# Kernel tuning notes

Hardware: AMD Instinct MI355X
Metric: run time of the kernel (lower is better)

The kernel has to match this reference:

```python
import jax, jax.numpy as jnp
import numpy as np

B, T, D, DFF, H, L, E, HID, GOUT = 64, 16, 2048, 2048, 8, 2, 32, 64, 32
THRESH = 0.05
MAXENT = float(np.log(7.0))

# per-sample edge template over 9 node slots: 0=phase, 1=location, 2..8=lesion k
_pairs = [(0, 1), (1, 0)]
for _k in range(7):
    _pairs += [(1, 2 + _k), (2 + _k, 1)]
for _i in range(7):
    for _j in range(_i + 1, 7):
        _pairs += [(2 + _i, 2 + _j), (2 + _j, 2 + _i)]
SRC_L = np.array([p[0] for p in _pairs], np.int32)  # [58]
DST_L = np.array([p[1] for p in _pairs], np.int32)


def _layernorm(x, g, b):
    m = x.mean(-1, keepdims=True)
    v = ((x - m) ** 2).mean(-1, keepdims=True)
    return (x - m) * jax.lax.rsqrt(v + 1e-5) * g + b


def setup_inputs():
    key = jax.random.key(0)
    ks = iter(jax.random.split(key, 32))
    def w(shape, s=0.02):
        return jax.random.normal(next(ks), shape, dtype=jnp.float32) * s
    return {
        'feat': jax.random.normal(next(ks), (B * T, D), dtype=jnp.float32),
        'w_phase': w((D, 3)), 'b_phase': jnp.zeros((3,), jnp.float32),
        'w_loc': w((D, 7)), 'b_loc': jnp.zeros((7,), jnp.float32),
        'w_les': w((D, 7)), 'b_les': jnp.zeros((7,), jnp.float32),
        'emb_phase': w((3, E), 1.0), 'emb_loc': w((7, E), 1.0),
        'les_emb_w': w((7, E), 0.2), 'les_emb_b': jnp.zeros((E,), jnp.float32),
        'qkv_w': w((L, 3 * D, D)), 'qkv_b': jnp.zeros((L, 3 * D), jnp.float32),
        'o_w': w((L, D, D)), 'o_b': jnp.zeros((L, D), jnp.float32),
        'ln1_g': jnp.ones((L, D), jnp.float32), 'ln1_b': jnp.zeros((L, D), jnp.float32),
        'ln2_g': jnp.ones((L, D), jnp.float32), 'ln2_b': jnp.zeros((L, D), jnp.float32),
        'ff1_w': w((L, DFF, D)), 'ff1_b': jnp.zeros((L, DFF), jnp.float32),
        'ff2_w': w((L, D, DFF)), 'ff2_b': jnp.zeros((L, D), jnp.float32),
        'w_score': w((D,)), 'b_score': jnp.zeros((1,), jnp.float32),
        'gcn1_w': w((E, HID), 0.2), 'gcn1_b': jnp.zeros((HID,), jnp.float32),
        'gcn2_w': w((HID, GOUT), 0.2), 'gcn2_b': jnp.zeros((GOUT,), jnp.float32),
        'w_diag': w((D + GOUT, 7)), 'b_diag': jnp.zeros((7,), jnp.float32),
        'mask': jax.random.randint(next(ks), (B, T), 0, 2, dtype=jnp.int32),
    }


def _forward(feat, w_phase, b_phase, w_loc, b_loc, w_les, b_les, emb_phase, emb_loc,
             les_emb_w, les_emb_b, qkv_w, qkv_b, o_w, o_b, ln1_g, ln1_b, ln2_g, ln2_b,
             ff1_w, ff1_b, ff2_w, ff2_b, w_score, b_score, gcn1_w, gcn1_b, gcn2_w,
             gcn2_b, w_diag, b_diag, mask):
    S = B * T
    Dh = D // H
    maskb = mask.astype(bool)            # [B,T]
    mflat = maskb.reshape(S)

    # per-frame heads
    phase_logits = feat @ w_phase + b_phase    # [S,3]
    loc_logits = feat @ w_loc + b_loc          # [S,7]
    les_logits = feat @ w_les + b_les          # [S,7]
    phase_ids = jnp.argmax(phase_logits, -1)
    loc_ids = jnp.argmax(loc_logits, -1)
    les_act = jax.nn.sigmoid(les_logits) > 0.5  # [S,7]

    # transformer encoder: 2 post-norm layers, eval mode (dropout off)
    x = feat.reshape(B, T, D)
    kp = maskb[:, None, None, :]
    for l in range(L):
        qkv = x @ qkv_w[l].T + qkv_b[l]
        q, k, v = jnp.split(qkv, 3, axis=-1)
        q = q.reshape(B, T, H, Dh)
        k = k.reshape(B, T, H, Dh)
        v = v.reshape(B, T, H, Dh)
        s = jnp.einsum('bqhd,bkhd->bhqk', q, k) / np.sqrt(Dh)
        s = jnp.where(kp, s, -1e9)
        a = jax.nn.softmax(s, axis=-1)
        ctx = jnp.einsum('bhqk,bkhd->bqhd', a, v).reshape(B, T, D)
        x = _layernorm(x + ctx @ o_w[l].T + o_b[l], ln1_g[l], ln1_b[l])
        ff = jax.nn.relu(x @ ff1_w[l].T + ff1_b[l]) @ ff2_w[l].T + ff2_b[l]
        x = _layernorm(x + ff, ln2_g[l], ln2_b[l])

    scores = x @ w_score + b_score             # [B,T]
    scores = jnp.where(maskb, scores, -jnp.inf)
    weights = jax.nn.softmax(scores, axis=1)
    pooled = jnp.einsum('btd,bt->bd', x, weights)

    # ---- graph build: 9 padded node slots per frame sample ----
    wflat = weights.reshape(S)
    valid = mflat & (wflat >= THRESH)
    node_mask = jnp.concatenate(
        [jnp.stack([valid, valid], 1), valid[:, None] & les_act], axis=1)  # [S,9]
    nodes = jnp.concatenate(
        [emb_phase[phase_ids][:, None], emb_loc[loc_ids][:, None],
         jnp.broadcast_to(les_emb_w + les_emb_b, (S, 7, E))], axis=1)      # [S,9,E]
    N = S * 9
    base = jnp.arange(S, dtype=jnp.int32)[:, None] * 9
    src = (base + SRC_L[None, :]).reshape(-1)
    dst = (base + DST_L[None, :]).reshape(-1)
    nm = node_mask.astype(jnp.float32)
    ew = (nm[:, SRC_L] * nm[:, DST_L]).reshape(-1)

    # temporal chain linking phase nodes of consecutive valid samples
    def _scan(carry, sv):
        s_i, v_i = sv
        nxt_i = carry
        carry = jnp.where(v_i, s_i, carry)
        return carry, nxt_i
    _, nxt = jax.lax.scan(_scan, jnp.int32(-1),
                          (jnp.arange(S, dtype=jnp.int32), valid), reverse=True)
    has_nxt = valid & (nxt >= 0)
    cs = jnp.arange(S, dtype=jnp.int32) * 9
    cd = jnp.maximum(nxt, 0) * 9
    cw = has_nxt.astype(jnp.float32)
    src = jnp.concatenate([src, cs, cd])
    dst = jnp.concatenate([dst, cd, cs])
    ew = jnp.concatenate([ew, cw, cw])

    # GCNConv: x' = D^{-1/2}(A+I)D^{-1/2} X W + b (self-loops included)
    def gcn(h, W, b):
        h = h @ W
        deg = jax.ops.segment_sum(ew, dst, num_segments=N) + 1.0
        dinv = jax.lax.rsqrt(deg)
        norm = dinv[src] * dinv[dst] * ew
        agg = jax.ops.segment_sum(norm[:, None] * h[src], dst, num_segments=N)
        return agg + h / deg[:, None] + b

    h = jax.nn.relu(gcn(nodes.reshape(N, E), gcn1_w, gcn1_b))
    h = jax.nn.relu(gcn(h, gcn2_w, gcn2_b)).reshape(S, 9, GOUT)

    # global_mean_pool per subgraph, then mean over a batch's subgraphs
    cnt = nm.sum(1)
    samp_mean = (h * nm[:, :, None]).sum(1) / jnp.maximum(cnt, 1.0)[:, None]  # [S,GOUT]
    vB = valid.reshape(B, T).astype(jnp.float32)
    gnn_pooled = jnp.einsum('btg,bt->bg', samp_mean.reshape(B, T, GOUT), vB) \
                 / jnp.maximum(vB.sum(1), 1.0)[:, None]

    diag_logits = jnp.concatenate([pooled, gnn_pooled], -1) @ w_diag + b_diag
    probs = jax.nn.softmax(diag_logits, -1)
    conf = probs.max(-1)
    ent = -(probs * jnp.log(probs + 1e-8)).sum(-1) / MAXENT
    return (phase_logits.reshape(B, T, 3), loc_logits.reshape(B, T, 7),
            les_logits.reshape(B, T, 7), diag_logits, conf, ent)


def reference(feat, w_phase, b_phase, w_loc, b_loc, w_les, b_les, emb_phase, emb_loc,
              les_emb_w, les_emb_b, qkv_w, qkv_b, o_w, o_b, ln1_g, ln1_b, ln2_g, ln2_b,
              ff1_w, ff1_b, ff2_w, ff2_b, w_score, b_score, gcn1_w, gcn1_b, gcn2_w,
              gcn2_b, w_diag, b_diag, mask):
    return _forward(feat, w_phase, b_phase, w_loc, b_loc, w_les, b_les, emb_phase,
                    emb_loc, les_emb_w, les_emb_b, qkv_w, qkv_b, o_w, o_b, ln1_g,
                    ln1_b, ln2_g, ln2_b, ff1_w, ff1_b, ff2_w, ff2_b, w_score, b_score,
                    gcn1_w, gcn1_b, gcn2_w, gcn2_b, w_diag, b_diag, mask)
```

## Files before the change

kernel.cpp:

```cpp
#include <hip/hip_runtime.h>
#include <hip/hip_bf16.h>
#include <math.h>

#define B_    64
#define T_    16
#define S_    1024
#define D_    2048
#define DFF_  2048
#define H_    8
#define DH_   256
#define L_    2
#define E_    32
#define HID_  64
#define GOUT_ 32
#define NN    (S_ * 9)

typedef unsigned short u16;
typedef float f32x4 __attribute__((ext_vector_type(4)));
typedef __bf16 bf16x8 __attribute__((ext_vector_type(8)));

__device__ __forceinline__ u16 f2bf_rne(float x) {
    union { float f; unsigned u; } c; c.f = x;
    unsigned u = c.u;
    unsigned r = (u + 0x7fffu + ((u >> 16) & 1u)) >> 16;
    return (u16)r;
}

__device__ __forceinline__ void gll16(const u16* g, u16* l) {
    __builtin_amdgcn_global_load_lds(
        (const __attribute__((address_space(1))) unsigned int*)g,
        (__attribute__((address_space(3))) unsigned int*)l,
        16, 0, 0);
}

__global__ __launch_bounds__(256)
void k_f2b(const float* __restrict__ in, u16* __restrict__ out, long n) {
    const long stride = (long)gridDim.x * 256 * 8;
    for (long i = ((long)blockIdx.x * 256 + threadIdx.x) * 8; i < n; i += stride) {
        const float4 a = *(const float4*)(in + i);
        const float4 b = *(const float4*)(in + i + 4);
        *(ushort4*)(out + i)     = make_ushort4(f2bf_rne(a.x), f2bf_rne(a.y),
                                                f2bf_rne(a.z), f2bf_rne(a.w));
        *(ushort4*)(out + i + 4) = make_ushort4(f2bf_rne(b.x), f2bf_rne(b.y),
                                                f2bf_rne(b.z), f2bf_rne(b.w));
    }
}

template<int EPI>
__global__ __launch_bounds__(256)
void gemm_bf(const u16* __restrict__ A, const u16* __restrict__ W,
             const float* __restrict__ bias, float* __restrict__ C,
             int N, int K, int KS) {
    __shared__ __align__(16) u16 As0[128 * 32];
    __shared__ __align__(16) u16 Bs0[128 * 32];
    __shared__ __align__(16) u16 As1[128 * 32];
    __shared__ __align__(16) u16 Bs1[128 * 32];
    const int tid  = threadIdx.x;
    const int lane = tid & 63;
    const int wv   = tid >> 6;
    const int wr   = wv >> 1, wc = wv & 1;
    const long m0 = (long)blockIdx.y * 128;
    const long n0 = (long)blockIdx.x * 128;
    const int kbase = blockIdx.z * KS;

    f32x4 acc[4][4];
#pragma unroll
    for (int i = 0; i < 4; i++)
#pragma unroll
        for (int j = 0; j < 4; j++)
#pragma unroll
            for (int r = 0; r < 4; r++) acc[i][j][r] = 0.0f;

    const int c0 = wv * 2, c1 = wv * 2 + 1;
    const int rsub = lane >> 2;
    const int kcol = (lane & 3) * 8;
    const u16* ga0 = A + (m0 + c0 * 16 + rsub) * (long)K + kbase + kcol;
    const u16* ga1 = A + (m0 + c1 * 16 + rsub) * (long)K + kbase + kcol;
    const u16* gb0 = W + (n0 + c0 * 16 + rsub) * (long)K + kbase + kcol;
    const u16* gb1 = W + (n0 + c1 * 16 + rsub) * (long)K + kbase + kcol;

    auto STAGE = [&](u16* dstA, u16* dstB) {
        gll16(ga0, dstA + c0 * 512);
        gll16(ga1, dstA + c1 * 512);
        gll16(gb0, dstB + c0 * 512);
        gll16(gb1, dstB + c1 * 512);
        ga0 += 32; ga1 += 32; gb0 += 32; gb1 += 32;
    };

    STAGE(As0, Bs0);
    __syncthreads();

    u16 *rA = As0, *rB = Bs0, *sA = As1, *sB = Bs1;
    const int nt = KS / 32;
    const int rbase = lane & 15;
    const int koff  = (lane >> 4) * 8;

    for (int t = 0; t < nt; ++t) {
        if (t + 1 < nt) STAGE(sA, sB);
        bf16x8 af[4], bfr[4];
#pragma unroll
        for (int i = 0; i < 4; i++) {
            af[i]  = *(const bf16x8*)&rA[(wr * 64 + i * 16 + rbase) * 32 + koff];
            bfr[i] = *(const bf16x8*)&rB[(wc * 64 + i * 16 + rbase) * 32 + koff];
        }
#pragma unroll
        for (int i = 0; i < 4; i++)
#pragma unroll
            for (int j = 0; j < 4; j++)
                acc[i][j] = __builtin_amdgcn_mfma_f32_16x16x32_bf16(af[i], bfr[j], acc[i][j], 0, 0, 0);
        __syncthreads();
        u16* t1 = rA; rA = sA; sA = t1;
        u16* t2 = rB; rB = sB; sB = t2;
    }

    float* Cout = (EPI == 1) ? (C + (long)blockIdx.z * ((long)S_ * N)) : C;
    const int crow = (lane >> 4) * 4;
    const int ccol = lane & 15;
#pragma unroll
    for (int i = 0; i < 4; i++) {
#pragma unroll
        for (int j = 0; j < 4; j++) {
            const long mb = m0 + wr * 64 + i * 16 + crow;
            const long nb = n0 + wc * 64 + j * 16 + ccol;
            float bv = 0.0f;
            if (EPI == 0) bv = bias[nb];
#pragma unroll
            for (int r = 0; r < 4; r++)
                Cout[(mb + r) * (long)N + nb] = acc[i][j][r] + bv;
        }
    }
}

__global__ __launch_bounds__(256)
void k_heads(const float* __restrict__ feat,
             const float* __restrict__ w_ph, const float* __restrict__ b_ph,
             const float* __restrict__ w_lc, const float* __restrict__ b_lc,
             const float* __restrict__ w_ls, const float* __restrict__ b_ls,
             float* __restrict__ o_ph, float* __restrict__ o_lc, float* __restrict__ o_ls,
             int* __restrict__ pid, int* __restrict__ lid, int* __restrict__ lesb) {
    const long s = blockIdx.x;
    const int tid = threadIdx.x;
    float a[17];
#pragma unroll
    for (int k = 0; k < 17; k++) a[k] = 0.0f;
    for (int d = tid; d < D_; d += 256) {
        const float f = feat[s * D_ + d];
        a[0] += f * w_ph[d * 3 + 0];
        a[1] += f * w_ph[d * 3 + 1];
        a[2] += f * w_ph[d * 3 + 2];
#pragma unroll
        for (int c = 0; c < 7; c++) a[3 + c]  += f * w_lc[d * 7 + c];
#pragma unroll
        for (int c = 0; c < 7; c++) a[10 + c] += f * w_ls[d * 7 + c];
    }
    __shared__ float red[4][17];
#pragma unroll
    for (int k = 0; k < 17; k++) {
        float v = a[k];
        for (int o = 32; o > 0; o >>= 1) v += __shfl_down(v, o, 64);
        if ((tid & 63) == 0) red[tid >> 6][k] = v;
    }
    __syncthreads();
    if (tid == 0) {
        float l[17];
#pragma unroll
        for (int k = 0; k < 17; k++) l[k] = red[0][k] + red[1][k] + red[2][k] + red[3][k];
        l[0] += b_ph[0]; l[1] += b_ph[1]; l[2] += b_ph[2];
#pragma unroll
        for (int c = 0; c < 7; c++) { l[3 + c] += b_lc[c]; l[10 + c] += b_ls[c]; }
        o_ph[s * 3 + 0] = l[0]; o_ph[s * 3 + 1] = l[1]; o_ph[s * 3 + 2] = l[2];
#pragma unroll
        for (int c = 0; c < 7; c++) { o_lc[s * 7 + c] = l[3 + c]; o_ls[s * 7 + c] = l[10 + c]; }
        int bp = 0;
        for (int j = 1; j < 3; j++) if (l[j] > l[bp]) bp = j;
        pid[s] = bp;
        int bl = 0;
        for (int c = 1; c < 7; c++) if (l[3 + c] > l[3 + bl]) bl = c;
        lid[s] = bl;
        int bits = 0;
        for (int c = 0; c < 7; c++) if (l[10 + c] > 0.0f) bits |= (1 << c);
        lesb[s] = bits;
    }
}

__global__ __launch_bounds__(256)
void k_attn(const float* __restrict__ qkv, const int* __restrict__ mask,
            u16* __restrict__ ctxb) {
    const int bh = blockIdx.x;
    const int b = bh >> 3, h = bh & 7;
    __shared__ float qs[16][257], ks[16][257], vs[16][257];
    __shared__ float sc[16][16];
    const int tid = threadIdx.x;
    for (int idx = tid; idx < 16 * 256; idx += 256) {
        const int t = idx >> 8, d = idx & 255;
        const long rb = ((long)(b * 16 + t)) * 6144 + h * 256 + d;
        qs[t][d] = qkv[rb];
        ks[t][d] = qkv[rb + 2048];
        vs[t][d] = qkv[rb + 4096];
    }
    __syncthreads();
    {
        const int i = tid >> 4, j = tid & 15;
        float dot = 0.0f;
        for (int d = 0; d < 256; d++) dot += qs[i][d] * ks[j][d];
        float sv = dot * (1.0f / 16.0f);
        if (mask[b * 16 + j] == 0) sv = -1000000000.0f;
        sc[i][j] = sv;
    }
    __syncthreads();
    if (tid < 16) {
        const int i = tid;
        float m = sc[i][0];
#pragma unroll
        for (int j = 1; j < 16; j++) m = fmaxf(m, sc[i][j]);
        float p[16], sum = 0.0f;
#pragma unroll
        for (int j = 0; j < 16; j++) { p[j] = expf(sc[i][j] - m); sum += p[j]; }
        const float inv = 1.0f / sum;
#pragma unroll
        for (int j = 0; j < 16; j++) sc[i][j] = p[j] * inv;
    }
    __syncthreads();
    {
        const int i = tid >> 4, c = tid & 15;
        float av[16];
#pragma unroll
        for (int j = 0; j < 16; j++) av[j] = sc[i][j];
#pragma unroll
        for (int o = 0; o < 16; o++) {
            const int d = o * 16 + c;
            float accv = 0.0f;
#pragma unroll
            for (int j = 0; j < 16; j++) accv += av[j] * vs[j][d];
            ctxb[((long)(b * 16 + i)) * 2048 + h * 256 + d] = f2bf_rne(accv);
        }
    }
}

__global__ __launch_bounds__(256)
void k_ln4(const float* __restrict__ xprev, const float* __restrict__ part,
           const float* __restrict__ pb, const float* __restrict__ g,
           const float* __restrict__ bt, float* __restrict__ outf,
           u16* __restrict__ outb) {
    __shared__ float buf[D_];
    __shared__ float red[8];
    const long s = blockIdx.x;
    const int tid = threadIdx.x;
    const long base = s * D_;
    const long P = (long)S_ * D_;
    float lsum = 0.0f;
    for (int d = tid; d < D_; d += 256) {
        const long i = base + d;
        const float v = xprev[i] + pb[d]
                      + part[i] + part[i + P] + part[i + 2 * P] + part[i + 3 * P];
        buf[d] = v;
        lsum += v;
    }
    for (int o = 32; o > 0; o >>= 1) lsum += __shfl_down(lsum, o, 64);
    if ((tid & 63) == 0) red[tid >> 6] = lsum;
    __syncthreads();
    const float mean = (red[0] + red[1] + red[2] + red[3]) * (1.0f / D_);
    float lvar = 0.0f;
    for (int d = tid; d < D_; d += 256) { const float dv = buf[d] - mean; lvar += dv * dv; }
    for (int o = 32; o > 0; o >>= 1) lvar += __shfl_down(lvar, o, 64);
    if ((tid & 63) == 0) red[4 + (tid >> 6)] = lvar;
    __syncthreads();
    const float var = (red[4] + red[5] + red[6] + red[7]) * (1.0f / D_);
    const float rstd = 1.0f / sqrtf(var + 1e-5f);
    for (int d = tid; d < D_; d += 256) {
        const float v = (buf[d] - mean) * rstd * g[d] + bt[d];
        outf[base + d] = v;
        outb[base + d] = f2bf_rne(v);
    }
}

__global__ __launch_bounds__(256)
void k_comb_relu(const float* __restrict__ part, const float* __restrict__ bias,
                 u16* __restrict__ outb) {
    const long i = ((long)blockIdx.x * 256 + threadIdx.x) * 4;
    const long P = (long)S_ * DFF_;
    const int n = (int)(i & (DFF_ - 1));
    float4 v  = *(const float4*)(part + i);
    const float4 v1 = *(const float4*)(part + i + P);
    const float4 v2 = *(const float4*)(part + i + 2 * P);
    const float4 v3 = *(const float4*)(part + i + 3 * P);
    const float4 bv = *(const float4*)(bias + n);
    v.x = fmaxf(v.x + v1.x + v2.x + v3.x + bv.x, 0.0f);
    v.y = fmaxf(v.y + v1.y + v2.y + v3.y + bv.y, 0.0f);
    v.z = fmaxf(v.z + v1.z + v2.z + v3.z + bv.z, 0.0f);
    v.w = fmaxf(v.w + v1.w + v2.w + v3.w + bv.w, 0.0f);
    *(ushort4*)(outb + i) = make_ushort4(f2bf_rne(v.x), f2bf_rne(v.y),
                                         f2bf_rne(v.z), f2bf_rne(v.w));
}

__global__ __launch_bounds__(256)
void k_scores(const float* __restrict__ x, const float* __restrict__ w,
              const float* __restrict__ bsc, float* __restrict__ scores) {
    const long s = blockIdx.x;
    const int tid = threadIdx.x;
    __shared__ float red[4];
    float a = 0.0f;
    for (int d = tid; d < D_; d += 256) a += x[s * D_ + d] * w[d];
    for (int o = 32; o > 0; o >>= 1) a += __shfl_down(a, o, 64);
    if ((tid & 63) == 0) red[tid >> 6] = a;
    __syncthreads();
    if (tid == 0) scores[s] = red[0] + red[1] + red[2] + red[3] + bsc[0];
}

__global__ void k_softT(const float* __restrict__ scores, const int* __restrict__ mask,
                        float* __restrict__ wts, int* __restrict__ validb) {
    const int b = blockIdx.x;
    const int t = threadIdx.x;
    float sv = -__builtin_inff();
    int mk = 0;
    if (t < 16) {
        mk = mask[b * 16 + t];
        sv = mk ? scores[b * 16 + t] : -__builtin_inff();
    }
    float m = sv;
    for (int o = 8; o > 0; o >>= 1) m = fmaxf(m, __shfl_xor(m, o, 16));
    float p = (t < 16) ? expf(sv - m) : 0.0f;
    float sum = p;
    for (int o = 8; o > 0; o >>= 1) sum += __shfl_xor(sum, o, 16);
    if (t < 16) {
        const float wv = p / sum;
        wts[b * 16 + t] = wv;
        validb[b * 16 + t] = (mk && (wv >= 0.05f)) ? 1 : 0;
    }
}

__global__ __launch_bounds__(256)
void k_pooled(const float* __restrict__ x, const float* __restrict__ wts,
              float* __restrict__ pooled) {
    const int b = blockIdx.y;
    const int d = blockIdx.x * 256 + threadIdx.x;
    float acc = 0.0f;
#pragma unroll
    for (int t = 0; t < 16; t++)
        acc += wts[b * 16 + t] * x[((long)(b * 16 + t)) * D_ + d];
    pooled[(long)b * D_ + d] = acc;
}

__global__ __launch_bounds__(1024)
void k_nxt(const int* __restrict__ validb, int* __restrict__ nxt,
           int* __restrict__ prevb, int* __restrict__ hasn) {
    __shared__ int v[S_], nx[S_], pv[S_];
    const int t = threadIdx.x;
    v[t] = validb[t];
    pv[t] = -1;
    __syncthreads();
    if (t == 0) {
        int carry = -1;
        for (int i = S_ - 1; i >= 0; i--) { nx[i] = carry; if (v[i]) carry = i; }
    }
    __syncthreads();
    const int h = (v[t] && nx[t] >= 0) ? 1 : 0;
    if (h) pv[nx[t]] = t;
    __syncthreads();
    nxt[t] = nx[t];
    hasn[t] = h;
    prevb[t] = pv[t];
}

__device__ __forceinline__ bool adj9(int u, int v) {
    if (u == v) return false;
    const int mn = u < v ? u : v;
    const int mx = u < v ? v : u;
    return !(mn == 0 && mx >= 2);
}

__global__ __launch_bounds__(64)
void k_deg(const int* __restrict__ validb, const int* __restrict__ lesb,
           const int* __restrict__ hasn, const int* __restrict__ prevb,
           float* __restrict__ deg, float* __restrict__ dinv) {
    const int s = blockIdx.x;
    const int t = threadIdx.x;
    __shared__ float nm[9];
    if (t < 9) {
        const int vl = validb[s];
        nm[t] = (t < 2) ? (vl ? 1.0f : 0.0f)
                        : ((vl && ((lesb[s] >> (t - 2)) & 1)) ? 1.0f : 0.0f);
    }
    __syncthreads();
    if (t < 9) {
        float dg = 1.0f;
        for (int u = 0; u < 9; u++)
            if (adj9(u, t)) dg += nm[u] * nm[t];
        if (t == 0) {
            dg += (float)hasn[s];
            if (prevb[s] >= 0) dg += 1.0f;
        }
        deg[s * 9 + t] = dg;
        dinv[s * 9 + t] = 1.0f / sqrtf(dg);
    }
}

__global__ __launch_bounds__(64)
void k_mm1(const int* __restrict__ pid, const int* __restrict__ lid,
           const float* __restrict__ embp, const float* __restrict__ embl,
           const float* __restrict__ lesw, const float* __restrict__ lesbv,
           const float* __restrict__ W1, float* __restrict__ h1pre) {
    const int s = blockIdx.x;
    const int t = threadIdx.x;
    __shared__ float nf[9][32];
    __shared__ float wl[32][64];
    for (int idx = t; idx < 9 * 32; idx += 64) {
        const int j = idx >> 5, e = idx & 31;
        float v;
        if (j == 0)      v = embp[pid[s] * 32 + e];
        else if (j == 1) v = embl[lid[s] * 32 + e];
        else             v = lesw[(j - 2) * 32 + e] + lesbv[e];
        nf[j][e] = v;
    }
    for (int idx = t; idx < 32 * 64; idx += 64) wl[idx >> 6][idx & 63] = W1[idx];
    __syncthreads();
    for (int j = 0; j < 9; j++) {
        float acc = 0.0f;
#pragma unroll
        for (int e = 0; e < 32; e++) acc += nf[j][e] * wl[e][t];
        h1pre[((long)(s * 9 + j)) * 64 + t] = acc;
    }
}

template<int F>
__global__ void k_agg(const float* __restrict__ hpre, const float* __restrict__ deg,
                      const float* __restrict__ dinv, const int* __restrict__ validb,
                      const int* __restrict__ lesb, const int* __restrict__ hasn,
                      const int* __restrict__ prevb, const int* __restrict__ nxt,
                      const float* __restrict__ bias, float* __restrict__ out) {
    const int s = blockIdx.x;
    const int t = threadIdx.x;
    __shared__ float hp[11][F];
    __shared__ float nm[9], di[11], dgo[9];
    for (int idx = t; idx < 11 * F; idx += F) {
        const int nl = idx / F, f = idx % F;
        float v = 0.0f;
        if (nl < 9) v = hpre[((long)(s * 9 + nl)) * F + f];
        else if (nl == 9)  { const int nx = nxt[s];  if (nx >= 0) v = hpre[((long)(nx * 9)) * F + f]; }
        else               { const int pb = prevb[s]; if (pb >= 0) v = hpre[((long)(pb * 9)) * F + f]; }
        hp[nl][f] = v;
    }
    if (t < 9) {
        const int vl = validb[s];
        nm[t] = (t < 2) ? (vl ? 1.0f : 0.0f)
                        : ((vl && ((lesb[s] >> (t - 2)) & 1)) ? 1.0f : 0.0f);
        di[t] = dinv[s * 9 + t];
        dgo[t] = deg[s * 9 + t];
    }
    if (t == 0) {
        const int nx = nxt[s];
        di[9]  = (nx >= 0) ? dinv[nx * 9] : 0.0f;
        const int pb = prevb[s];
        di[10] = (pb >= 0) ? dinv[pb * 9] : 0.0f;
    }
    __syncthreads();
    const float wn = (float)hasn[s];
    const float wp = (prevb[s] >= 0) ? 1.0f : 0.0f;
    for (int j = 0; j < 9; j++) {
        float acc = hp[j][t] / dgo[j] + bias[t];
        const float djj = di[j], nmj = nm[j];
        for (int u = 0; u < 9; u++)
            if (adj9(u, j)) acc += di[u] * djj * nm[u] * nmj * hp[u][t];
        if (j == 0) {
            acc += di[9]  * djj * wn * hp[9][t];
            acc += di[10] * djj * wp * hp[10][t];
        }
        out[((long)(s * 9 + j)) * F + t] = fmaxf(acc, 0.0f);
    }
}

__global__ __launch_bounds__(64)
void k_mm2(const float* __restrict__ h1, const float* __restrict__ W2,
           float* __restrict__ h2pre) {
    const int s = blockIdx.x;
    const int t = threadIdx.x;
    __shared__ float hf[9][64];
    __shared__ float wl[64][32];
    for (int idx = t; idx < 9 * 64; idx += 64) hf[idx >> 6][idx & 63] = h1[(long)s * 9 * 64 + idx];
    for (int idx = t; idx < 64 * 32; idx += 64) wl[idx >> 5][idx & 31] = W2[idx];
    __syncthreads();
    const int o = t & 31, jh = t >> 5;
    for (int j = jh; j < 9; j += 2) {
        float acc = 0.0f;
#pragma unroll
        for (int e = 0; e < 64; e++) acc += hf[j][e] * wl[e][o];
        h2pre[((long)(s * 9 + j)) * 32 + o] = acc;
    }
}

__global__ void k_sampgnn(const float* __restrict__ h2, const int* __restrict__ validb,
                          const int* __restrict__ lesb, float* __restrict__ gnnp) {
    const int b = blockIdx.x;
    const int t = threadIdx.x;
    float acc = 0.0f, vcnt = 0.0f;
    for (int tt = 0; tt < 16; tt++) {
        const int s = b * 16 + tt;
        if (validb[s]) {
            const int lb = lesb[s];
            float cnt = 2.0f;
            float sm = h2[((long)(s * 9 + 0)) * 32 + t] + h2[((long)(s * 9 + 1)) * 32 + t];
#pragma unroll
            for (int k = 0; k < 7; k++) {
                if ((lb >> k) & 1) { cnt += 1.0f; sm += h2[((long)(s * 9 + 2 + k)) * 32 + t]; }
            }
            acc += sm / fmaxf(cnt, 1.0f);
            vcnt += 1.0f;
        }
    }
    gnnp[b * 32 + t] = acc / fmaxf(vcnt, 1.0f);
}

__global__ __launch_bounds__(256)
void k_diag(const float* __restrict__ pooled, const float* __restrict__ gnnp,
            const float* __restrict__ wd, const float* __restrict__ bd,
            float* __restrict__ o_dg, float* __restrict__ o_cf, float* __restrict__ o_en) {
    const int b = blockIdx.x;
    const int tid = threadIdx.x;
    float a[7];
#pragma unroll
    for (int c = 0; c < 7; c++) a[c] = 0.0f;
    for (int d = tid; d < 2080; d += 256) {
        const float v = (d < 2048) ? pooled[(long)b * 2048 + d] : gnnp[b * 32 + (d - 2048)];
#pragma unroll
        for (int c = 0; c < 7; c++) a[c] += v * wd[d * 7 + c];
    }
    __shared__ float red[4][7];
#pragma unroll
    for (int c = 0; c < 7; c++) {
        float v = a[c];
        for (int o = 32; o > 0; o >>= 1) v += __shfl_down(v, o, 64);
        if ((tid & 63) == 0) red[tid >> 6][c] = v;
    }
    __syncthreads();
    if (tid == 0) {
        float l[7];
        float m = -__builtin_inff();
#pragma unroll
        for (int c = 0; c < 7; c++) {
            l[c] = red[0][c] + red[1][c] + red[2][c] + red[3][c] + bd[c];
            o_dg[b * 7 + c] = l[c];
            m = fmaxf(m, l[c]);
        }
        float p[7], sum = 0.0f;
#pragma unroll
        for (int c = 0; c < 7; c++) { p[c] = expf(l[c] - m); sum += p[c]; }
        const float inv = 1.0f / sum;
        float conf = 0.0f, ent = 0.0f;
#pragma unroll
        for (int c = 0; c < 7; c++) {
            const float pr = p[c] * inv;
            conf = fmaxf(conf, pr);
            ent -= pr * logf(pr + 1e-8f);
        }
        o_cf[b] = conf;
        o_en[b] = ent * (1.0f / 1.9459101090932196f);
    }
}

extern "C" void kernel_launch(void* const* d_in, const int* in_sizes, int n_in,
                              void* d_out, int out_size, void* d_ws, size_t ws_size,
                              hipStream_t stream) {
    const float* feat      = (const float*)d_in[0];
    const float* w_phase   = (const float*)d_in[1];
    const float* b_phase   = (const float*)d_in[2];
    const float* w_loc     = (const float*)d_in[3];
    const float* b_loc     = (const float*)d_in[4];
    const float* w_les     = (const float*)d_in[5];
    const float* b_les     = (const float*)d_in[6];
    const float* emb_phase = (const float*)d_in[7];
    const float* emb_loc   = (const float*)d_in[8];
    const float* les_emb_w = (const float*)d_in[9];
    const float* les_emb_b = (const float*)d_in[10];
    const float* qkv_w     = (const float*)d_in[11];
    const float* qkv_b     = (const float*)d_in[12];
    const float* o_w       = (const float*)d_in[13];
    const float* o_b       = (const float*)d_in[14];
    const float* ln1_g     = (const float*)d_in[15];
    const float* ln1_b     = (const float*)d_in[16];
    const float* ln2_g     = (const float*)d_in[17];
    const float* ln2_b     = (const float*)d_in[18];
    const float* ff1_w     = (const float*)d_in[19];
    const float* ff1_b     = (const float*)d_in[20];
    const float* ff2_w     = (const float*)d_in[21];
    const float* ff2_b     = (const float*)d_in[22];
    const float* w_score   = (const float*)d_in[23];
    const float* b_score   = (const float*)d_in[24];
    const float* gcn1_w    = (const float*)d_in[25];
    const float* gcn1_b    = (const float*)d_in[26];
    const float* gcn2_w    = (const float*)d_in[27];
    const float* gcn2_b    = (const float*)d_in[28];
    const float* w_diag    = (const float*)d_in[29];
    const float* b_diag    = (const float*)d_in[30];
    const int*   mask      = (const int*)d_in[31];

    float* out  = (float*)d_out;
    float* o_ph = out;
    float* o_lc = out + 3072;
    float* o_ls = out + 10240;
    float* o_dg = out + 17408;
    float* o_cf = out + 17856;
    float* o_en = out + 17920;

    float* w = (float*)d_ws;
    float* x      = w; w += (long)S_ * D_;
    float* pbuf   = w; w += 4L * S_ * 2048;
    float* qkvb   = pbuf;
    float* scores = w; w += S_;
    float* wts    = w; w += S_;
    float* pooled = w; w += (long)B_ * D_;
    float* h1pre  = w; w += (long)NN * HID_;
    float* h1     = w; w += (long)NN * HID_;
    float* h2pre  = w; w += (long)NN * GOUT_;
    float* h2     = w; w += (long)NN * GOUT_;
    float* degv   = w; w += NN;
    float* dinvv  = w; w += NN;
    float* gnnp   = w; w += B_ * GOUT_;
    int* ivs    = (int*)w;
    int* pid    = ivs;
    int* lid    = ivs + S_;
    int* lesb   = ivs + 2 * S_;
    int* validb = ivs + 3 * S_;
    int* nxtb   = ivs + 4 * S_;
    int* prevb  = ivs + 5 * S_;
    int* hasn   = ivs + 6 * S_;
    u16* ub   = (u16*)(ivs + 7 * S_);
    u16* featb = ub; ub += (long)S_ * D_;
    u16* xb    = ub; ub += (long)S_ * D_;
    u16* ctxb  = ub; ub += (long)S_ * D_;
    u16* ffbb  = ub; ub += (long)S_ * DFF_;
    u16* wbuf  = ub; ub += 3L * D_ * D_;

    k_heads<<<S_, 256, 0, stream>>>(feat, w_phase, b_phase, w_loc, b_loc, w_les, b_les,
                                    o_ph, o_lc, o_ls, pid, lid, lesb);
    k_f2b<<<2048, 256, 0, stream>>>(feat, featb, (long)S_ * D_);

    const float* xinf = feat;
    const u16*   xinb = featb;
    for (int l = 0; l < L_; l++) {
        k_f2b<<<2048, 256, 0, stream>>>(qkv_w + (long)l * 3 * D_ * D_, wbuf, 3L * D_ * D_);
        gemm_bf<0><<<dim3(48, 8, 1), 256, 0, stream>>>(
            xinb, wbuf, qkv_b + (long)l * 3 * D_, qkvb, 3 * D_, D_, D_);
        k_attn<<<B_ * H_, 256, 0, stream>>>(qkvb, mask, ctxb);
        k_f2b<<<2048, 256, 0, stream>>>(o_w + (long)l * D_ * D_, wbuf, (long)D_ * D_);
        gemm_bf<1><<<dim3(16, 8, 4), 256, 0, stream>>>(
            ctxb, wbuf, nullptr, pbuf, D_, D_, D_ / 4);
        k_ln4<<<S_, 256, 0, stream>>>(xinf, pbuf, o_b + (long)l * D_,
                                      ln1_g + (long)l * D_, ln1_b + (long)l * D_, x, xb);
        k_f2b<<<2048, 256, 0, stream>>>(ff1_w + (long)l * DFF_ * D_, wbuf, (long)DFF_ * D_);
        gemm_bf<1><<<dim3(16, 8, 4), 256, 0, stream>>>(
            xb, wbuf, nullptr, pbuf, DFF_, D_, D_ / 4);
        k_comb_relu<<<2048, 256, 0, stream>>>(pbuf, ff1_b + (long)l * DFF_, ffbb);
        k_f2b<<<2048, 256, 0, stream>>>(ff2_w + (long)l * D_ * DFF_, wbuf, (long)D_ * DFF_);
        gemm_bf<1><<<dim3(16, 8, 4), 256, 0, stream>>>(
            ffbb, wbuf, nullptr, pbuf, D_, DFF_, DFF_ / 4);
        k_ln4<<<S_, 256, 0, stream>>>(x, pbuf, ff2_b + (long)l * D_,
                                      ln2_g + (long)l * D_, ln2_b + (long)l * D_, x, xb);
        xinf = x;
        xinb = xb;
    }

    k_scores<<<S_, 256, 0, stream>>>(x, w_score, b_score, scores);
    k_softT<<<B_, 64, 0, stream>>>(scores, mask, wts, validb);
    k_pooled<<<dim3(8, B_), 256, 0, stream>>>(x, wts, pooled);
    k_nxt<<<1, 1024, 0, stream>>>(validb, nxtb, prevb, hasn);
    k_deg<<<S_, 64, 0, stream>>>(validb, lesb, hasn, prevb, degv, dinvv);
    k_mm1<<<S_, 64, 0, stream>>>(pid, lid, emb_phase, emb_loc, les_emb_w, les_emb_b, gcn1_w, h1pre);
    k_agg<64><<<S_, 64, 0, stream>>>(h1pre, degv, dinvv, validb, lesb, hasn, prevb, nxtb, gcn1_b, h1);
    k_mm2<<<S_, 64, 0, stream>>>(h1, gcn2_w, h2pre);
    k_agg<32><<<S_, 32, 0, stream>>>(h2pre, degv, dinvv, validb, lesb, hasn, prevb, nxtb, gcn2_b, h2);
    k_sampgnn<<<B_, 32, 0, stream>>>(h2, validb, lesb, gnnp);
    k_diag<<<B_, 256, 0, stream>>>(pooled, gnnp, w_diag, b_diag, o_dg, o_cf, o_en);
}
```

Baseline: 675.9 us.

## Split-K the QKV GEMM and remap workgroups across XCDs

```diff
diff --git a/kernel.cpp b/kernel.cpp
--- a/kernel.cpp
+++ b/kernel.cpp
@@ -46,11 +46,9 @@
     }
 }
 
-template<int EPI>
 __global__ __launch_bounds__(256)
 void gemm_bf(const u16* __restrict__ A, const u16* __restrict__ W,
-             const float* __restrict__ bias, float* __restrict__ C,
-             int N, int K, int KS) {
+             float* __restrict__ C, int N, int K, int KS) {
     __shared__ __align__(16) u16 As0[128 * 32];
     __shared__ __align__(16) u16 Bs0[128 * 32];
     __shared__ __align__(16) u16 As1[128 * 32];
@@ -59,9 +57,19 @@
     const int lane = tid & 63;
     const int wv   = tid >> 6;
     const int wr   = wv >> 1, wc = wv & 1;
-    const long m0 = (long)blockIdx.y * 128;
-    const long n0 = (long)blockIdx.x * 128;
-    const int kbase = blockIdx.z * KS;
+
+    const int gx = gridDim.x, gy = gridDim.y, gz = gridDim.z;
+    int id = blockIdx.x + gx * (blockIdx.y + gy * blockIdx.z);
+    const int nwg = gx * gy * gz;
+    id = (id & 7) * (nwg >> 3) + (id >> 3);
+    const int bx = id % gx;
+    const int tq = id / gx;
+    const int by = tq % gy;
+    const int bz = tq / gy;
+
+    const long m0 = (long)by * 128;
+    const long n0 = (long)bx * 128;
+    const int kbase = bz * KS;
 
     f32x4 acc[4][4];
 #pragma unroll
@@ -113,7 +121,7 @@
         u16* t2 = rB; rB = sB; sB = t2;
     }
 
-    float* Cout = (EPI == 1) ? (C + (long)blockIdx.z * ((long)S_ * N)) : C;
+    float* Cout = C + (long)bz * ((long)S_ * N);
     const int crow = (lane >> 4) * 4;
     const int ccol = lane & 15;
 #pragma unroll
@@ -122,11 +130,9 @@
         for (int j = 0; j < 4; j++) {
             const long mb = m0 + wr * 64 + i * 16 + crow;
             const long nb = n0 + wc * 64 + j * 16 + ccol;
-            float bv = 0.0f;
-            if (EPI == 0) bv = bias[nb];
 #pragma unroll
             for (int r = 0; r < 4; r++)
-                Cout[(mb + r) * (long)N + nb] = acc[i][j][r] + bv;
+                Cout[(mb + r) * (long)N + nb] = acc[i][j][r];
         }
     }
 }
@@ -184,19 +190,21 @@
 }
 
 __global__ __launch_bounds__(256)
-void k_attn(const float* __restrict__ qkv, const int* __restrict__ mask,
-            u16* __restrict__ ctxb) {
+void k_attn(const float* __restrict__ part, const float* __restrict__ qb,
+            const int* __restrict__ mask, u16* __restrict__ ctxb) {
     const int bh = blockIdx.x;
     const int b = bh >> 3, h = bh & 7;
     __shared__ float qs[16][257], ks[16][257], vs[16][257];
     __shared__ float sc[16][16];
     const int tid = threadIdx.x;
+    const long P6 = (long)S_ * 6144;
     for (int idx = tid; idx < 16 * 256; idx += 256) {
         const int t = idx >> 8, d = idx & 255;
         const long rb = ((long)(b * 16 + t)) * 6144 + h * 256 + d;
-        qs[t][d] = qkv[rb];
-        ks[t][d] = qkv[rb + 2048];
-        vs[t][d] = qkv[rb + 4096];
+        const int cb = h * 256 + d;
+        qs[t][d] = part[rb]        + part[rb + P6]        + qb[cb];
+        ks[t][d] = part[rb + 2048] + part[rb + 2048 + P6] + qb[cb + 2048];
+        vs[t][d] = part[rb + 4096] + part[rb + 4096 + P6] + qb[cb + 4096];
     }
     __syncthreads();
     {
@@ -603,8 +611,7 @@
 
     float* w = (float*)d_ws;
     float* x      = w; w += (long)S_ * D_;
-    float* pbuf   = w; w += 4L * S_ * 2048;
-    float* qkvb   = pbuf;
+    float* pbuf   = w; w += 2L * S_ * 6144;
     float* scores = w; w += S_;
     float* wts    = w; w += S_;
     float* pooled = w; w += (long)B_ * D_;
@@ -638,21 +645,17 @@
     const u16*   xinb = featb;
     for (int l = 0; l < L_; l++) {
         k_f2b<<<2048, 256, 0, stream>>>(qkv_w + (long)l * 3 * D_ * D_, wbuf, 3L * D_ * D_);
-        gemm_bf<0><<<dim3(48, 8, 1), 256, 0, stream>>>(
-            xinb, wbuf, qkv_b + (long)l * 3 * D_, qkvb, 3 * D_, D_, D_);
-        k_attn<<<B_ * H_, 256, 0, stream>>>(qkvb, mask, ctxb);
+        gemm_bf<<<dim3(48, 8, 2), 256, 0, stream>>>(xinb, wbuf, pbuf, 3 * D_, D_, D_ / 2);
+        k_attn<<<B_ * H_, 256, 0, stream>>>(pbuf, qkv_b + (long)l * 3 * D_, mask, ctxb);
         k_f2b<<<2048, 256, 0, stream>>>(o_w + (long)l * D_ * D_, wbuf, (long)D_ * D_);
-        gemm_bf<1><<<dim3(16, 8, 4), 256, 0, stream>>>(
-            ctxb, wbuf, nullptr, pbuf, D_, D_, D_ / 4);
+        gemm_bf<<<dim3(16, 8, 4), 256, 0, stream>>>(ctxb, wbuf, pbuf, D_, D_, D_ / 4);
         k_ln4<<<S_, 256, 0, stream>>>(xinf, pbuf, o_b + (long)l * D_,
                                       ln1_g + (long)l * D_, ln1_b + (long)l * D_, x, xb);
         k_f2b<<<2048, 256, 0, stream>>>(ff1_w + (long)l * DFF_ * D_, wbuf, (long)DFF_ * D_);
-        gemm_bf<1><<<dim3(16, 8, 4), 256, 0, stream>>>(
-            xb, wbuf, nullptr, pbuf, DFF_, D_, D_ / 4);
+        gemm_bf<<<dim3(16, 8, 4), 256, 0, stream>>>(xb, wbuf, pbuf, DFF_, D_, D_ / 4);
         k_comb_relu<<<2048, 256, 0, stream>>>(pbuf, ff1_b + (long)l * DFF_, ffbb);
         k_f2b<<<2048, 256, 0, stream>>>(ff2_w + (long)l * D_ * DFF_, wbuf, (long)D_ * DFF_);
-        gemm_bf<1><<<dim3(16, 8, 4), 256, 0, stream>>>(
-            ffbb, wbuf, nullptr, pbuf, D_, DFF_, DFF_ / 4);
+        gemm_bf<<<dim3(16, 8, 4), 256, 0, stream>>>(ffbb, wbuf, pbuf, D_, DFF_, DFF_ / 4);
         k_ln4<<<S_, 256, 0, stream>>>(x, pbuf, ff2_b + (long)l * D_,
                                       ln2_g + (long)l * D_, ln2_b + (long)l * D_, x, xb);
         xinf = x;
```

After: 664.9 us. Within noise of the previous version (-1.6%).
